# Optimization experiments

Measured on AMD Instinct MI355X. Metric: run time of the kernel, lower is better.

The kernel has to match this reference:

```python
import jax, jax.numpy as jnp
import numpy as np

B, S, D = 1, 2048, 1024
L, H, NH = 256, 1024, 16  # latent_dim, hidden_dim, num_heads
HD = H // NH
EPS = 1e-6


def rmsnorm(x, g):
    return x * jax.lax.rsqrt(jnp.mean(x * x, axis=-1, keepdims=True) + EPS) * g


def setup_inputs() -> dict:
    key = jax.random.key(0)
    ks = jax.random.split(key, 16)
    def w(k, shape, fan_in):
        return jax.random.normal(k, shape, jnp.float32) / np.sqrt(fan_in)
    return {
        "x": jax.random.normal(ks[0], (B, S, D), jnp.float32),
        "g1": jnp.ones((D,), jnp.float32),
        "Wq": w(ks[1], (D, H), D), "bq": jnp.zeros((H,), jnp.float32),
        "Wdown": w(ks[2], (D, L), D), "bdown": jnp.zeros((L,), jnp.float32),
        "Wk": w(ks[3], (L, H), L), "bk": jnp.zeros((H,), jnp.float32),
        "Wv": w(ks[4], (L, H), L), "bv": jnp.zeros((H,), jnp.float32),
        "Wo": w(ks[5], (H, D), H), "bo": jnp.zeros((D,), jnp.float32),
        "g2": jnp.ones((D,), jnp.float32),
        "W1": w(ks[6], (D, 4 * D), D), "b1": jnp.zeros((4 * D,), jnp.float32),
        "W2": w(ks[7], (4 * D, D), 4 * D), "b2": jnp.zeros((D,), jnp.float32),
    }


def reference(x, g1, Wq, bq, Wdown, bdown, Wk, bk, Wv, bv, Wo, bo, g2, W1, b1, W2, b2):
    stream = x
    # RMSNorm -> MLA (low-rank latent KV attention, causal)
    h = rmsnorm(x, g1)
    q = (h @ Wq + bq).reshape(B, S, NH, HD)
    c = h @ Wdown + bdown                       # [B,S,L] compressed KV latent
    k = (c @ Wk + bk).reshape(B, S, NH, HD)
    v = (c @ Wv + bv).reshape(B, S, NH, HD)
    scores = jnp.einsum("bqhd,bkhd->bhqk", q, k) / np.sqrt(HD)
    causal = jnp.tril(jnp.ones((S, S), bool))
    scores = jnp.where(causal, scores, jnp.finfo(scores.dtype).min)
    attn = jax.nn.softmax(scores, axis=-1)
    o = jnp.einsum("bhqk,bkhd->bqhd", attn, v).reshape(B, S, H)
    stream = (o @ Wo + bo) + stream
    # RMSNorm -> FFN (D -> 4D -> D, activation on every layer incl. last)
    h = rmsnorm(stream, g2)
    h = jax.nn.silu(h @ W1 + b1)
    h = jax.nn.silu(h @ W2 + b2)
    return h + stream
```

## Files before the change

### kernel.cpp

```cpp
#include <hip/hip_runtime.h>

typedef __bf16 bf16x8 __attribute__((ext_vector_type(8)));
typedef float  f32x4  __attribute__((ext_vector_type(4)));

static __device__ __forceinline__ ushort f2bf(float f) {
    union { float f; unsigned u; } a; a.f = f;
    unsigned r = a.u + 0x7FFFu + ((a.u >> 16) & 1u);
    return (ushort)(r >> 16);
}
static __device__ __forceinline__ ushort f2bf_hw(float f) {
    __bf16 b = (__bf16)f;
    return __builtin_bit_cast(ushort, b);
}
static __device__ __forceinline__ float bf2f(ushort u) {
    return __builtin_bit_cast(float, (unsigned)u << 16);
}

#define TS  2048
#define TD  1024
#define TL  256
#define TH  1024
#define TNH 16
#define THD 64
#define TDF 4096
#define ATT_CE 0.18033688f
#define NSPLIT 4

#define GLD_LDS(gp, lp) \
    __builtin_amdgcn_global_load_lds( \
        (const __attribute__((address_space(1))) unsigned int*)(gp), \
        (__attribute__((address_space(3))) unsigned int*)(lp), 16, 0, 0)

__device__ __forceinline__ void transpose_body(
    const float* __restrict__ in, ushort* __restrict__ out,
    int K, int N, int bK, int bN, int tid, float (*tile)[33])
{
    const int k0 = bK * 32, n0 = bN * 32;
    const int tx = tid & 31, ty = tid >> 5;
#pragma unroll
    for (int i = ty; i < 32; i += 8)
        tile[i][tx] = in[(size_t)(k0 + i) * N + n0 + tx];
    __syncthreads();
#pragma unroll
    for (int i = ty; i < 32; i += 8)
        out[(size_t)(n0 + i) * K + k0 + tx] = f2bf(tile[tx][i]);
}

__global__ __launch_bounds__(256) void prep_kernel(
    const float* __restrict__ x, const float* __restrict__ g1,
    const float* __restrict__ Wq, const float* __restrict__ Wdown,
    const float* __restrict__ Wk, const float* __restrict__ Wv,
    const float* __restrict__ Wo, const float* __restrict__ W1,
    const float* __restrict__ W2,
    const float* __restrict__ bk, const float* __restrict__ bv,
    ushort* __restrict__ WqT, ushort* __restrict__ WdownT,
    ushort* __restrict__ WkvT, ushort* __restrict__ WoT,
    ushort* __restrict__ W1T, ushort* __restrict__ W2T,
    float* __restrict__ bkv, ushort* __restrict__ hbuf)
{
    __shared__ float tile[32][33];
    __shared__ float sums[4];
    int b = blockIdx.x;
    const int tid = threadIdx.x;
    if (b < 1024) {
        transpose_body(Wq, WqT, TD, TH, b & 31, b >> 5, tid, tile);
    } else if (b < 1280) {
        b -= 1024;
        transpose_body(Wdown, WdownT, TD, TL, b & 31, b >> 5, tid, tile);
    } else if (b < 1536) {
        b -= 1280;
        transpose_body(Wk, WkvT, TL, TH, b & 7, b >> 3, tid, tile);
    } else if (b < 1792) {
        b -= 1536;
        transpose_body(Wv, WkvT + (size_t)TH * TL, TL, TH, b & 7, b >> 3, tid, tile);
    } else if (b < 2816) {
        b -= 1792;
        transpose_body(Wo, WoT, TH, TD, b & 31, b >> 5, tid, tile);
    } else if (b < 6912) {
        b -= 2816;
        transpose_body(W1, W1T, TD, TDF, b & 31, b >> 5, tid, tile);
    } else if (b < 11008) {
        b -= 6912;
        transpose_body(W2, W2T, TDF, TD, b & 127, b >> 7, tid, tile);
    } else if (b < 11016) {
        b -= 11008;
        const int i = b * 256 + tid;
        bkv[i] = (i < TH) ? bk[i] : bv[i - TH];
    } else {
        const int row = b - 11016;
        const float4 v = ((const float4*)(x + (size_t)row * TD))[tid];
        float ss = v.x * v.x + v.y * v.y + v.z * v.z + v.w * v.w;
#pragma unroll
        for (int off = 32; off > 0; off >>= 1) ss += __shfl_down(ss, off);
        if ((tid & 63) == 0) sums[tid >> 6] = ss;
        __syncthreads();
        const float tot = sums[0] + sums[1] + sums[2] + sums[3];
        const float scale = rsqrtf(tot / (float)TD + 1e-6f);
        const float4 gv = ((const float4*)g1)[tid];
        ushort4 o;
        o.x = f2bf(v.x * scale * gv.x);
        o.y = f2bf(v.y * scale * gv.y);
        o.z = f2bf(v.z * scale * gv.z);
        o.w = f2bf(v.w * scale * gv.w);
        *(ushort4*)(hbuf + (size_t)row * TD + tid * 4) = o;
    }
}

__global__ __launch_bounds__(256) void rmsnorm_kernel(
    const float* __restrict__ x, const float* __restrict__ g,
    ushort* __restrict__ out, int D)
{
    const int row = blockIdx.x;
    const int tid = threadIdx.x;
    const float4 v = ((const float4*)(x + (size_t)row * D))[tid];
    float ss = v.x * v.x + v.y * v.y + v.z * v.z + v.w * v.w;
#pragma unroll
    for (int off = 32; off > 0; off >>= 1) ss += __shfl_down(ss, off);
    __shared__ float sums[4];
    if ((tid & 63) == 0) sums[tid >> 6] = ss;
    __syncthreads();
    const float tot = sums[0] + sums[1] + sums[2] + sums[3];
    const float scale = rsqrtf(tot / (float)D + 1e-6f);
    const float4 gv = ((const float4*)g)[tid];
    ushort4 o;
    o.x = f2bf(v.x * scale * gv.x);
    o.y = f2bf(v.y * scale * gv.y);
    o.z = f2bf(v.z * scale * gv.z);
    o.w = f2bf(v.w * scale * gv.w);
    *(ushort4*)(out + (size_t)row * D + tid * 4) = o;
}

template <int EPI, int BM, int BN, int BKH>
__global__ __launch_bounds__(256) void gemm_bf16_kernel(
    const ushort* __restrict__ A, const ushort* __restrict__ BT,
    const float* __restrict__ bias, const float* __restrict__ resid,
    void* __restrict__ outp, int M, int N, int K)
{
    constexpr int WM = BM / 2, WN = BN / 2;
    constexpr int MT = WM / 16, NT = WN / 16;
    constexpr int NLA = BM / 64, NLB = BN / 64;
    __shared__ alignas(16) ushort As[2][BKH][BM * 32];
    __shared__ alignas(16) ushort Bs[2][BKH][BN * 32];
    const int bm = blockIdx.y * BM, bn = blockIdx.x * BN;
    const int tid = threadIdx.x;
    const int lane = tid & 63, wave = tid >> 6;
    const int wr = (wave >> 1) * WM, wc = (wave & 1) * WN;
    const int l15 = lane & 15, l4 = lane >> 4;

    f32x4 acc[MT][NT] = {};

    const int grow = wave * 16 + (lane >> 2);
    const int gcol = (lane & 3) * 8;
    const ushort* Ag = A + (size_t)(bm + grow) * K + gcol;
    const ushort* Bg = BT + (size_t)(bn + grow) * K + gcol;

    auto stage = [&](int buf, int k0) {
#pragma unroll
        for (int h = 0; h < BKH; ++h) {
#pragma unroll
            for (int i = 0; i < NLA; ++i)
                GLD_LDS(Ag + (size_t)(i * 64) * K + k0 + h * 32,
                        &As[buf][h][(i * 64 + wave * 16) * 32]);
#pragma unroll
            for (int i = 0; i < NLB; ++i)
                GLD_LDS(Bg + (size_t)(i * 64) * K + k0 + h * 32,
                        &Bs[buf][h][(i * 64 + wave * 16) * 32]);
        }
    };

    stage(0, 0);
    asm volatile("s_waitcnt vmcnt(0)" ::: "memory");
    __syncthreads();

    const int nsteps = K / (32 * BKH);
    for (int t = 0; t < nsteps; ++t) {
        const int cur = t & 1;
        if (t + 1 < nsteps) stage(cur ^ 1, (t + 1) * 32 * BKH);

#pragma unroll
        for (int h = 0; h < BKH; ++h) {
            bf16x8 af[MT], bf[NT];
#pragma unroll
            for (int mt = 0; mt < MT; ++mt)
                af[mt] = *(const bf16x8*)&As[cur][h][(wr + mt * 16 + l15) * 32 + l4 * 8];
#pragma unroll
            for (int nt = 0; nt < NT; ++nt)
                bf[nt] = *(const bf16x8*)&Bs[cur][h][(wc + nt * 16 + l15) * 32 + l4 * 8];
#pragma unroll
            for (int mt = 0; mt < MT; ++mt)
#pragma unroll
                for (int nt = 0; nt < NT; ++nt)
                    acc[mt][nt] = __builtin_amdgcn_mfma_f32_16x16x32_bf16(
                        af[mt], bf[nt], acc[mt][nt], 0, 0, 0);
        }

        asm volatile("s_waitcnt vmcnt(0)" ::: "memory");
        __syncthreads();
    }

#pragma unroll
    for (int mt = 0; mt < MT; ++mt) {
#pragma unroll
        for (int nt = 0; nt < NT; ++nt) {
#pragma unroll
            for (int i = 0; i < 4; ++i) {
                const int row = bm + wr + mt * 16 + l4 * 4 + i;
                const int col = bn + wc + nt * 16 + l15;
                float v = acc[mt][nt][i] + bias[col];
                if constexpr (EPI == 1 || EPI == 3) v = v / (1.f + __expf(-v));
                if constexpr (EPI == 2 || EPI == 3) v += resid[(size_t)row * N + col];
                if constexpr (EPI == 0 || EPI == 1)
                    ((ushort*)outp)[(size_t)row * N + col] = f2bf(v);
                else
                    ((float*)outp)[(size_t)row * N + col] = v;
            }
        }
    }
}

__global__ __launch_bounds__(256) void mla_attn_kernel(
    const ushort* __restrict__ Q, const ushort* __restrict__ Kg,
    const ushort* __restrict__ Vg, ushort* __restrict__ OP, float* __restrict__ ML)
{
    constexpr int QSTR = 1024, KSTR = 2048;
    __shared__ alignas(16) ushort Ks[2][64 * 64];
    __shared__ alignas(16) ushort VTs[2][64 * 64];
    __shared__ alignas(16) ushort Ps[4][16 * 64];
    const int qb = (int)gridDim.x - 1 - (int)blockIdx.x;
    const int h = blockIdx.y;
    const int sp = blockIdx.z;
    const int tid = threadIdx.x, lane = tid & 63, wave = tid >> 6;
    const int l15 = lane & 15, l4 = lane >> 4;
    const int qrow0 = qb * 64 + wave * 16;
    const int myq = qrow0 + l15;

    const int ntile = qb + 1;
    const int chunk = (ntile + NSPLIT - 1) / NSPLIT;
    const int kt0 = sp * chunk;
    const int ktend = min(ntile, kt0 + chunk);

    auto swzK = [](ushort* base, int row, int colbyte) -> ushort* {
        return (ushort*)((char*)base + row * 128 + (colbyte ^ ((row & 7) << 4)));
    };
    auto swzVT = [](ushort* base, int d, int colbyte) -> ushort* {
        return (ushort*)((char*)base + d * 128 + (colbyte ^ (((d >> 3) & 7) << 4)));
    };
    auto swzP = [&](int row, int colbyte) -> ushort* {
        return (ushort*)((char*)&Ps[wave][0] + row * 128 + (colbyte ^ ((row & 7) << 4)));
    };

    bf16x8 qf[2];
#pragma unroll
    for (int ks = 0; ks < 2; ++ks)
        qf[ks] = *(const bf16x8*)&Q[(size_t)(qrow0 + l15) * QSTR + h * THD + ks * 32 + l4 * 8];

    f32x4 oacc[4] = {};
    float m_run = -1e30f, l_run = 0.f;

    const int sr = tid >> 3, sc = (tid & 7) * 8;
    const ushort* kbase = Kg + (size_t)sr * KSTR + h * THD + sc;
    const ushort* vbase = Vg + (size_t)sr * KSTR + h * THD + sc;

    uint4 kr0, kr1, vr0, vr1;
    if (kt0 < ktend) {
        {
            const size_t off = (size_t)kt0 * 64 * KSTR;
            kr0 = *(const uint4*)(kbase + off);
            kr1 = *(const uint4*)(kbase + off + (size_t)32 * KSTR);
            vr0 = *(const uint4*)(vbase + off);
            vr1 = *(const uint4*)(vbase + off + (size_t)32 * KSTR);
            *(uint4*)swzK(&Ks[0][0], sr, sc * 2) = kr0;
            *(uint4*)swzK(&Ks[0][0], sr + 32, sc * 2) = kr1;
            const ushort* p0 = (const ushort*)&vr0;
            const ushort* p1 = (const ushort*)&vr1;
#pragma unroll
            for (int j = 0; j < 8; ++j) {
                *swzVT(&VTs[0][0], sc + j, sr * 2) = p0[j];
                *swzVT(&VTs[0][0], sc + j, (sr + 32) * 2) = p1[j];
            }
        }
        if (kt0 + 1 < ktend) {
            const size_t off = (size_t)(kt0 + 1) * 64 * KSTR;
            kr0 = *(const uint4*)(kbase + off);
            kr1 = *(const uint4*)(kbase + off + (size_t)32 * KSTR);
            vr0 = *(const uint4*)(vbase + off);
            vr1 = *(const uint4*)(vbase + off + (size_t)32 * KSTR);
        }
    }

    for (int kt = kt0; kt < ktend; ++kt) {
        const int rel = kt - kt0;
        __syncthreads();
        if (kt + 1 < ktend) {
            ushort* kd = &Ks[(rel + 1) & 1][0];
            ushort* vd = &VTs[(rel + 1) & 1][0];
            *(uint4*)swzK(kd, sr, sc * 2) = kr0;
            *(uint4*)swzK(kd, sr + 32, sc * 2) = kr1;
            const ushort* p0 = (const ushort*)&vr0;
            const ushort* p1 = (const ushort*)&vr1;
#pragma unroll
            for (int j = 0; j < 8; ++j) {
                *swzVT(vd, sc + j, sr * 2) = p0[j];
                *swzVT(vd, sc + j, (sr + 32) * 2) = p1[j];
            }
            if (kt + 2 < ktend) {
                const size_t off = (size_t)(kt + 2) * 64 * KSTR;
                kr0 = *(const uint4*)(kbase + off);
                kr1 = *(const uint4*)(kbase + off + (size_t)32 * KSTR);
                vr0 = *(const uint4*)(vbase + off);
                vr1 = *(const uint4*)(vbase + off + (size_t)32 * KSTR);
            }
        }
        const ushort* kb_lds = &Ks[rel & 1][0];
        const ushort* vb_lds = &VTs[rel & 1][0];

        f32x4 s[4] = {};
        __builtin_amdgcn_s_setprio(1);
#pragma unroll
        for (int ks = 0; ks < 2; ++ks) {
#pragma unroll
            for (int nt = 0; nt < 4; ++nt) {
                const bf16x8 kf = *(const bf16x8*)swzK((ushort*)kb_lds, nt * 16 + l15, ks * 64 + l4 * 16);
                s[nt] = __builtin_amdgcn_mfma_f32_16x16x32_bf16(kf, qf[ks], s[nt], 0, 0, 0);
            }
        }
        __builtin_amdgcn_s_setprio(0);

        if (kt == qb) {
            const int kb = kt * 64;
#pragma unroll
            for (int nt = 0; nt < 4; ++nt)
#pragma unroll
                for (int i = 0; i < 4; ++i)
                    if (kb + nt * 16 + l4 * 4 + i > myq) s[nt][i] = -3.0e38f;
        }

        float mx = m_run;
#pragma unroll
        for (int nt = 0; nt < 4; ++nt)
#pragma unroll
            for (int i = 0; i < 4; ++i) mx = fmaxf(mx, s[nt][i]);
        mx = fmaxf(mx, __shfl_xor(mx, 16));
        mx = fmaxf(mx, __shfl_xor(mx, 32));
        const float alpha = exp2f((m_run - mx) * ATT_CE);
        m_run = mx;
        float ps = 0.f;
#pragma unroll
        for (int nt = 0; nt < 4; ++nt)
#pragma unroll
            for (int i = 0; i < 4; ++i) {
                const float p = exp2f((s[nt][i] - mx) * ATT_CE);
                s[nt][i] = p;
                ps += p;
            }
        ps += __shfl_xor(ps, 16);
        ps += __shfl_xor(ps, 32);
        l_run = l_run * alpha + ps;

#pragma unroll
        for (int dt = 0; dt < 4; ++dt)
#pragma unroll
            for (int i = 0; i < 4; ++i) oacc[dt][i] *= alpha;

#pragma unroll
        for (int nt = 0; nt < 4; ++nt) {
            ushort4 pk;
            pk.x = f2bf_hw(s[nt][0]); pk.y = f2bf_hw(s[nt][1]);
            pk.z = f2bf_hw(s[nt][2]); pk.w = f2bf_hw(s[nt][3]);
            *(ushort4*)swzP(l15, nt * 32 + l4 * 8) = pk;
        }

        __builtin_amdgcn_s_setprio(1);
#pragma unroll
        for (int ks = 0; ks < 2; ++ks) {
            const bf16x8 pf = *(const bf16x8*)swzP(l15, ks * 64 + l4 * 16);
#pragma unroll
            for (int dt = 0; dt < 4; ++dt) {
                const bf16x8 vf = *(const bf16x8*)swzVT((ushort*)vb_lds, dt * 16 + l15, ks * 64 + l4 * 16);
                oacc[dt] = __builtin_amdgcn_mfma_f32_16x16x32_bf16(vf, pf, oacc[dt], 0, 0, 0);
            }
        }
        __builtin_amdgcn_s_setprio(0);
    }

    ushort* op = OP + (size_t)sp * TS * TH;
#pragma unroll
    for (int dt = 0; dt < 4; ++dt) {
        ushort4 o4;
        o4.x = f2bf_hw(oacc[dt][0]); o4.y = f2bf_hw(oacc[dt][1]);
        o4.z = f2bf_hw(oacc[dt][2]); o4.w = f2bf_hw(oacc[dt][3]);
        *(ushort4*)&op[(size_t)myq * TH + h * THD + dt * 16 + l4 * 4] = o4;
    }
    if (l4 == 0) {
        float* ml = ML + (size_t)sp * TS * TNH * 2;
        ml[((size_t)myq * TNH + h) * 2 + 0] = m_run;
        ml[((size_t)myq * TNH + h) * 2 + 1] = l_run;
    }
}

__global__ __launch_bounds__(256) void attn_combine_kernel(
    const ushort* __restrict__ OP, const float* __restrict__ ML,
    ushort* __restrict__ O)
{
    const int idx = blockIdx.x * 256 + threadIdx.x;
    const int row = idx >> 8;
    const int h = (idx & 255) >> 4;
    float m[NSPLIT], l[NSPLIT];
#pragma unroll
    for (int sp = 0; sp < NSPLIT; ++sp) {
        m[sp] = ML[((size_t)sp * TS * TNH + (size_t)row * TNH + h) * 2 + 0];
        l[sp] = ML[((size_t)sp * TS * TNH + (size_t)row * TNH + h) * 2 + 1];
    }
    float M = m[0];
#pragma unroll
    for (int sp = 1; sp < NSPLIT; ++sp) M = fmaxf(M, m[sp]);
    float w[NSPLIT], den = 0.f;
#pragma unroll
    for (int sp = 0; sp < NSPLIT; ++sp) {
        w[sp] = exp2f((m[sp] - M) * ATT_CE);
        den += l[sp] * w[sp];
    }
    const float inv = 1.f / den;
    float ax = 0.f, ay = 0.f, az = 0.f, aw = 0.f;
#pragma unroll
    for (int sp = 0; sp < NSPLIT; ++sp) {
        const ushort4 u = ((const ushort4*)(OP + (size_t)sp * TS * TH))[idx];
        ax += w[sp] * bf2f(u.x);
        ay += w[sp] * bf2f(u.y);
        az += w[sp] * bf2f(u.z);
        aw += w[sp] * bf2f(u.w);
    }
    ushort4 o;
    o.x = f2bf_hw(ax * inv);
    o.y = f2bf_hw(ay * inv);
    o.z = f2bf_hw(az * inv);
    o.w = f2bf_hw(aw * inv);
    ((ushort4*)O)[idx] = o;
}

extern "C" void kernel_launch(void* const* d_in, const int* in_sizes, int n_in,
                              void* d_out, int out_size, void* d_ws, size_t ws_size,
                              hipStream_t stream)
{
    const float* x     = (const float*)d_in[0];
    const float* g1    = (const float*)d_in[1];
    const float* Wq    = (const float*)d_in[2];
    const float* bq    = (const float*)d_in[3];
    const float* Wdown = (const float*)d_in[4];
    const float* bdown = (const float*)d_in[5];
    const float* Wk    = (const float*)d_in[6];
    const float* bk    = (const float*)d_in[7];
    const float* Wv    = (const float*)d_in[8];
    const float* bv    = (const float*)d_in[9];
    const float* Wo    = (const float*)d_in[10];
    const float* bo    = (const float*)d_in[11];
    const float* g2    = (const float*)d_in[12];
    const float* W1    = (const float*)d_in[13];
    const float* b1    = (const float*)d_in[14];
    const float* W2    = (const float*)d_in[15];
    const float* b2    = (const float*)d_in[16];
    float* out = (float*)d_out;

    char* ws = (char*)d_ws;
    size_t off = 0;
    auto alloc = [&](size_t bytes) {
        void* p = ws + off;
        off += (bytes + 255) & ~(size_t)255;
        return p;
    };
    ushort* WqT    = (ushort*)alloc((size_t)TH * TD * 2);
    ushort* WdownT = (ushort*)alloc((size_t)TL * TD * 2);
    ushort* WkvT   = (ushort*)alloc((size_t)2 * TH * TL * 2);
    ushort* WoT    = (ushort*)alloc((size_t)TD * TH * 2);
    ushort* W1T    = (ushort*)alloc((size_t)TDF * TD * 2);
    ushort* W2T    = (ushort*)alloc((size_t)TD * TDF * 2);
    float*  bkv    = (float*)alloc((size_t)2 * TH * 4);
    ushort* hbuf   = (ushort*)alloc((size_t)TS * TD * 2);
    ushort* cbuf   = (ushort*)alloc((size_t)TS * TL * 2);
    ushort* qbuf   = (ushort*)alloc((size_t)TS * TH * 2);
    ushort* kvbuf  = (ushort*)alloc((size_t)TS * 2 * TH * 2);
    ushort* obuf   = (ushort*)alloc((size_t)TS * TH * 2);
    float*  strm   = (float*)alloc((size_t)TS * TD * 4);
    ushort* h2buf  = (ushort*)alloc((size_t)TS * TD * 2);
    ushort* ffn1   = (ushort*)alloc((size_t)TS * TDF * 2);
    float*  mlbuf  = (float*)alloc((size_t)NSPLIT * TS * TNH * 2 * 4);
    ushort* opart  = (ushort*)ffn1;

    prep_kernel<<<13064, 256, 0, stream>>>(
        x, g1, Wq, Wdown, Wk, Wv, Wo, W1, W2, bk, bv,
        WqT, WdownT, WkvT, WoT, W1T, W2T, bkv, hbuf);

    gemm_bf16_kernel<0, 64, 64, 2><<<dim3(TH / 64, TS / 64), 256, 0, stream>>>(
        hbuf, WqT, bq, nullptr, qbuf, TS, TH, TD);
    gemm_bf16_kernel<0, 64, 64, 2><<<dim3(TL / 64, TS / 64), 256, 0, stream>>>(
        hbuf, WdownT, bdown, nullptr, cbuf, TS, TL, TD);
    gemm_bf16_kernel<0, 64, 64, 2><<<dim3(2 * TH / 64, TS / 64), 256, 0, stream>>>(
        cbuf, WkvT, bkv, nullptr, kvbuf, TS, 2 * TH, TL);

    mla_attn_kernel<<<dim3(TS / 64, TNH, NSPLIT), 256, 0, stream>>>(
        qbuf, kvbuf, kvbuf + TH, opart, mlbuf);
    attn_combine_kernel<<<(TS * TH / 4) / 256, 256, 0, stream>>>(
        opart, mlbuf, obuf);

    gemm_bf16_kernel<2, 64, 64, 2><<<dim3(TD / 64, TS / 64), 256, 0, stream>>>(
        obuf, WoT, bo, x, strm, TS, TD, TH);

    rmsnorm_kernel<<<TS, 256, 0, stream>>>(strm, g2, h2buf, TD);

    gemm_bf16_kernel<1, 64, 64, 2><<<dim3(TDF / 64, TS / 64), 256, 0, stream>>>(
        h2buf, W1T, b1, nullptr, ffn1, TS, TDF, TD);
    gemm_bf16_kernel<3, 64, 64, 2><<<dim3(TD / 64, TS / 64), 256, 0, stream>>>(
        ffn1, W2T, b2, strm, out, TS, TD, TDF);
}
```

Baseline: 198.8 us.

## Fuse Q and down projections into one GEMM and split-K the W2 GEMM

Concatenates Wq and Wdown (and their biases) into a single transposed weight, so one GEMM produces both q and the latent c in a strided buffer. The KV GEMM and attention read from that buffer through a new lda parameter. The W2 GEMM, which has a long K of 4096 and only 512 tiles, is split into two K halves that write fp32 partial sums. A new combine kernel then adds the halves with bias, applies SiLU and adds the residual. This is meant to cut a launch and raise occupancy on the tail GEMM, at the cost of an extra 16MB of partial-sum traffic and one more kernel.

```diff
diff --git a/kernel.cpp b/kernel.cpp
--- a/kernel.cpp
+++ b/kernel.cpp
@@ -23,6 +23,7 @@
 #define TNH 16
 #define THD 64
 #define TDF 4096
+#define TQC 1280
 #define ATT_CE 0.18033688f
 #define NSPLIT 4
 
@@ -52,21 +53,23 @@
     const float* __restrict__ Wk, const float* __restrict__ Wv,
     const float* __restrict__ Wo, const float* __restrict__ W1,
     const float* __restrict__ W2,
+    const float* __restrict__ bq, const float* __restrict__ bdown,
     const float* __restrict__ bk, const float* __restrict__ bv,
-    ushort* __restrict__ WqT, ushort* __restrict__ WdownT,
-    ushort* __restrict__ WkvT, ushort* __restrict__ WoT,
-    ushort* __restrict__ W1T, ushort* __restrict__ W2T,
-    float* __restrict__ bkv, ushort* __restrict__ hbuf)
+    ushort* __restrict__ WqdT, ushort* __restrict__ WkvT,
+    ushort* __restrict__ WoT, ushort* __restrict__ W1T,
+    ushort* __restrict__ W2T,
+    float* __restrict__ bkv, float* __restrict__ bqd,
+    ushort* __restrict__ hbuf)
 {
     __shared__ float tile[32][33];
     __shared__ float sums[4];
     int b = blockIdx.x;
     const int tid = threadIdx.x;
     if (b < 1024) {
-        transpose_body(Wq, WqT, TD, TH, b & 31, b >> 5, tid, tile);
+        transpose_body(Wq, WqdT, TD, TH, b & 31, b >> 5, tid, tile);
     } else if (b < 1280) {
         b -= 1024;
-        transpose_body(Wdown, WdownT, TD, TL, b & 31, b >> 5, tid, tile);
+        transpose_body(Wdown, WqdT + (size_t)TH * TD, TD, TL, b & 31, b >> 5, tid, tile);
     } else if (b < 1536) {
         b -= 1280;
         transpose_body(Wk, WkvT, TL, TH, b & 7, b >> 3, tid, tile);
@@ -86,8 +89,12 @@
         b -= 11008;
         const int i = b * 256 + tid;
         bkv[i] = (i < TH) ? bk[i] : bv[i - TH];
+    } else if (b < 11021) {
+        b -= 11016;
+        const int i = b * 256 + tid;
+        if (i < TQC) bqd[i] = (i < TH) ? bq[i] : bdown[i - TH];
     } else {
-        const int row = b - 11016;
+        const int row = b - 11021;
         const float4 v = ((const float4*)(x + (size_t)row * TD))[tid];
         float ss = v.x * v.x + v.y * v.y + v.z * v.z + v.w * v.w;
 #pragma unroll
@@ -130,11 +137,11 @@
     *(ushort4*)(out + (size_t)row * D + tid * 4) = o;
 }
 
-template <int EPI, int BM, int BN, int BKH>
+template <int EPI, int BM, int BN, int BKH, int NKS>
 __global__ __launch_bounds__(256) void gemm_bf16_kernel(
     const ushort* __restrict__ A, const ushort* __restrict__ BT,
     const float* __restrict__ bias, const float* __restrict__ resid,
-    void* __restrict__ outp, int M, int N, int K)
+    void* __restrict__ outp, int M, int N, int K, int lda)
 {
     constexpr int WM = BM / 2, WN = BN / 2;
     constexpr int MT = WM / 16, NT = WN / 16;
@@ -147,19 +154,22 @@
     const int wr = (wave >> 1) * WM, wc = (wave & 1) * WN;
     const int l15 = lane & 15, l4 = lane >> 4;
 
+    const int Kblk = K / NKS;
+    const int kbeg = (NKS > 1) ? (int)blockIdx.z * Kblk : 0;
+
     f32x4 acc[MT][NT] = {};
 
     const int grow = wave * 16 + (lane >> 2);
     const int gcol = (lane & 3) * 8;
-    const ushort* Ag = A + (size_t)(bm + grow) * K + gcol;
-    const ushort* Bg = BT + (size_t)(bn + grow) * K + gcol;
+    const ushort* Ag = A + (size_t)(bm + grow) * lda + gcol + kbeg;
+    const ushort* Bg = BT + (size_t)(bn + grow) * K + gcol + kbeg;
 
     auto stage = [&](int buf, int k0) {
 #pragma unroll
         for (int h = 0; h < BKH; ++h) {
 #pragma unroll
             for (int i = 0; i < NLA; ++i)
-                GLD_LDS(Ag + (size_t)(i * 64) * K + k0 + h * 32,
+                GLD_LDS(Ag + (size_t)(i * 64) * lda + k0 + h * 32,
                         &As[buf][h][(i * 64 + wave * 16) * 32]);
 #pragma unroll
             for (int i = 0; i < NLB; ++i)
@@ -172,7 +182,7 @@
     asm volatile("s_waitcnt vmcnt(0)" ::: "memory");
     __syncthreads();
 
-    const int nsteps = K / (32 * BKH);
+    const int nsteps = Kblk / (32 * BKH);
     for (int t = 0; t < nsteps; ++t) {
         const int cur = t & 1;
         if (t + 1 < nsteps) stage(cur ^ 1, (t + 1) * 32 * BKH);
@@ -206,23 +216,45 @@
             for (int i = 0; i < 4; ++i) {
                 const int row = bm + wr + mt * 16 + l4 * 4 + i;
                 const int col = bn + wc + nt * 16 + l15;
-                float v = acc[mt][nt][i] + bias[col];
+                float v = acc[mt][nt][i];
+                if constexpr (EPI != 4) v += bias[col];
                 if constexpr (EPI == 1 || EPI == 3) v = v / (1.f + __expf(-v));
                 if constexpr (EPI == 2 || EPI == 3) v += resid[(size_t)row * N + col];
                 if constexpr (EPI == 0 || EPI == 1)
                     ((ushort*)outp)[(size_t)row * N + col] = f2bf(v);
+                else if constexpr (EPI == 4)
+                    ((float*)outp)[(size_t)blockIdx.z * M * N + (size_t)row * N + col] = v;
                 else
                     ((float*)outp)[(size_t)row * N + col] = v;
             }
         }
     }
+}
+
+__global__ __launch_bounds__(256) void w2_combine_kernel(
+    const float* __restrict__ P, const float* __restrict__ bias,
+    const float* __restrict__ resid, float* __restrict__ out)
+{
+    const int idx = blockIdx.x * 256 + threadIdx.x;
+    const int c4 = idx & (TD / 4 - 1);
+    const float4 p0 = ((const float4*)P)[idx];
+    const float4 p1 = ((const float4*)(P + (size_t)TS * TD))[idx];
+    const float4 bb = ((const float4*)bias)[c4];
+    const float4 rr = ((const float4*)resid)[idx];
+    float4 o;
+    float v;
+    v = p0.x + p1.x + bb.x; o.x = v / (1.f + __expf(-v)) + rr.x;
+    v = p0.y + p1.y + bb.y; o.y = v / (1.f + __expf(-v)) + rr.y;
+    v = p0.z + p1.z + bb.z; o.z = v / (1.f + __expf(-v)) + rr.z;
+    v = p0.w + p1.w + bb.w; o.w = v / (1.f + __expf(-v)) + rr.w;
+    ((float4*)out)[idx] = o;
 }
 
 __global__ __launch_bounds__(256) void mla_attn_kernel(
     const ushort* __restrict__ Q, const ushort* __restrict__ Kg,
     const ushort* __restrict__ Vg, ushort* __restrict__ OP, float* __restrict__ ML)
 {
-    constexpr int QSTR = 1024, KSTR = 2048;
+    constexpr int QSTR = TQC, KSTR = 2048;
     __shared__ alignas(16) ushort Ks[2][64 * 64];
     __shared__ alignas(16) ushort VTs[2][64 * 64];
     __shared__ alignas(16) ushort Ps[4][16 * 64];
@@ -468,47 +500,48 @@
         off += (bytes + 255) & ~(size_t)255;
         return p;
     };
-    ushort* WqT    = (ushort*)alloc((size_t)TH * TD * 2);
-    ushort* WdownT = (ushort*)alloc((size_t)TL * TD * 2);
+    ushort* WqdT   = (ushort*)alloc((size_t)TQC * TD * 2);
     ushort* WkvT   = (ushort*)alloc((size_t)2 * TH * TL * 2);
     ushort* WoT    = (ushort*)alloc((size_t)TD * TH * 2);
     ushort* W1T    = (ushort*)alloc((size_t)TDF * TD * 2);
     ushort* W2T    = (ushort*)alloc((size_t)TD * TDF * 2);
     float*  bkv    = (float*)alloc((size_t)2 * TH * 4);
+    float*  bqd    = (float*)alloc((size_t)TQC * 4);
     ushort* hbuf   = (ushort*)alloc((size_t)TS * TD * 2);
-    ushort* cbuf   = (ushort*)alloc((size_t)TS * TL * 2);
-    ushort* qbuf   = (ushort*)alloc((size_t)TS * TH * 2);
+    ushort* qcbuf  = (ushort*)alloc((size_t)TS * TQC * 2);
     ushort* kvbuf  = (ushort*)alloc((size_t)TS * 2 * TH * 2);
     ushort* obuf   = (ushort*)alloc((size_t)TS * TH * 2);
     float*  strm   = (float*)alloc((size_t)TS * TD * 4);
     ushort* h2buf  = (ushort*)alloc((size_t)TS * TD * 2);
     ushort* ffn1   = (ushort*)alloc((size_t)TS * TDF * 2);
     float*  mlbuf  = (float*)alloc((size_t)NSPLIT * TS * TNH * 2 * 4);
+    float*  psum   = (float*)alloc((size_t)2 * TS * TD * 4);
     ushort* opart  = (ushort*)ffn1;
 
-    prep_kernel<<<13064, 256, 0, stream>>>(
-        x, g1, Wq, Wdown, Wk, Wv, Wo, W1, W2, bk, bv,
-        WqT, WdownT, WkvT, WoT, W1T, W2T, bkv, hbuf);
-
-    gemm_bf16_kernel<0, 64, 64, 2><<<dim3(TH / 64, TS / 64), 256, 0, stream>>>(
-        hbuf, WqT, bq, nullptr, qbuf, TS, TH, TD);
-    gemm_bf16_kernel<0, 64, 64, 2><<<dim3(TL / 64, TS / 64), 256, 0, stream>>>(
-        hbuf, WdownT, bdown, nullptr, cbuf, TS, TL, TD);
-    gemm_bf16_kernel<0, 64, 64, 2><<<dim3(2 * TH / 64, TS / 64), 256, 0, stream>>>(
-        cbuf, WkvT, bkv, nullptr, kvbuf, TS, 2 * TH, TL);
+    prep_kernel<<<13069, 256, 0, stream>>>(
+        x, g1, Wq, Wdown, Wk, Wv, Wo, W1, W2, bq, bdown, bk, bv,
+        WqdT, WkvT, WoT, W1T, W2T, bkv, bqd, hbuf);
+
+    gemm_bf16_kernel<0, 64, 64, 2, 1><<<dim3(TQC / 64, TS / 64), 256, 0, stream>>>(
+        hbuf, WqdT, bqd, nullptr, qcbuf, TS, TQC, TD, TD);
+    gemm_bf16_kernel<0, 64, 64, 2, 1><<<dim3(2 * TH / 64, TS / 64), 256, 0, stream>>>(
+        qcbuf + TH, WkvT, bkv, nullptr, kvbuf, TS, 2 * TH, TL, TQC);
 
     mla_attn_kernel<<<dim3(TS / 64, TNH, NSPLIT), 256, 0, stream>>>(
-        qbuf, kvbuf, kvbuf + TH, opart, mlbuf);
+        qcbuf, kvbuf, kvbuf + TH, opart, mlbuf);
     attn_combine_kernel<<<(TS * TH / 4) / 256, 256, 0, stream>>>(
         opart, mlbuf, obuf);
 
-    gemm_bf16_kernel<2, 64, 64, 2><<<dim3(TD / 64, TS / 64), 256, 0, stream>>>(
-        obuf, WoT, bo, x, strm, TS, TD, TH);
+    gemm_bf16_kernel<2, 64, 64, 2, 1><<<dim3(TD / 64, TS / 64), 256, 0, stream>>>(
+        obuf, WoT, bo, x, strm, TS, TD, TH, TH);
 
     rmsnorm_kernel<<<TS, 256, 0, stream>>>(strm, g2, h2buf, TD);
 
-    gemm_bf16_kernel<1, 64, 64, 2><<<dim3(TDF / 64, TS / 64), 256, 0, stream>>>(
-        h2buf, W1T, b1, nullptr, ffn1, TS, TDF, TD);
-    gemm_bf16_kernel<3, 64, 64, 2><<<dim3(TD / 64, TS / 64), 256, 0, stream>>>(
-        ffn1, W2T, b2, strm, out, TS, TD, TDF);
-}
+    gemm_bf16_kernel<1, 64, 64, 2, 1><<<dim3(TDF / 64, TS / 64), 256, 0, stream>>>(
+        h2buf, W1T, b1, nullptr, ffn1, TS, TDF, TD, TD);
+
+    gemm_bf16_kernel<4, 64, 64, 2, 2><<<dim3(TD / 64, TS / 64, 2), 256, 0, stream>>>(
+        ffn1, W2T, nullptr, nullptr, psum, TS, TD, TDF, TDF);
+    w2_combine_kernel<<<(TS * TD / 4) / 256, 256, 0, stream>>>(
+        psum, b2, strm, out);
+}
```

Measured after the change: 187.6 us. 1.06x faster.
